# Optimization experiments

Measured on AMD Instinct MI355X. Metric: run time of the kernel, lower is better.

The kernel has to match this reference:

```python
import jax, jax.numpy as jnp
import numpy as np

EMBED_DIM = 256
NUM_HEADS = 4
HEAD_DIM = EMBED_DIM // NUM_HEADS  # 64
FEAT_X = FEAT_Y = 64               # 64*64 = 4096 tokens
THETA = 10000.0


def _axial_cos_sin(dim, end_x, end_y, theta):
    # compute_axial_cis: dim//4 frequencies per spatial axis, concatenated -> [N, dim//2]
    f = 1.0 / (theta ** (np.arange(0, dim, 4)[: dim // 4].astype(np.float32) / dim))
    t = np.arange(end_x * end_y)
    tx = (t % end_x).astype(np.float32)
    ty = (t // end_x).astype(np.float32)
    ang = np.concatenate([np.outer(tx, f), np.outer(ty, f)], axis=-1)  # [N, dim//2]
    return jnp.asarray(np.cos(ang)), jnp.asarray(np.sin(ang))


def _apply_rope(x, cos, sin):
    # x: [B, H, N, D]; adjacent pairs (x[..., 2i], x[..., 2i+1]) are the complex parts
    xr = x.reshape(*x.shape[:-1], -1, 2)
    xa, xb = xr[..., 0], xr[..., 1]          # [B, H, N, D//2]
    oa = xa * cos - xb * sin                  # cos/sin: [N, D//2], broadcast
    ob = xa * sin + xb * cos
    return jnp.stack([oa, ob], axis=-1).reshape(x.shape)


def setup_inputs() -> dict:
    key = jax.random.key(0)
    ks = jax.random.split(key, 8)
    B, N, D = 1, FEAT_X * FEAT_Y, EMBED_DIM
    s = 0.02  # weight init scale
    return {
        "q": jax.random.normal(ks[0], (B, N, D), jnp.float32),
        "k": jax.random.normal(ks[1], (B, N, D), jnp.float32),
        "v": jax.random.normal(ks[2], (B, N, D), jnp.float32),
        "wq": jax.random.normal(ks[3], (D, D), jnp.float32) * s,
        "bq": jnp.zeros((D,), jnp.float32),
        "wk": jax.random.normal(ks[4], (D, D), jnp.float32) * s,
        "bk": jnp.zeros((D,), jnp.float32),
        "wv": jax.random.normal(ks[5], (D, D), jnp.float32) * s,
        "bv": jnp.zeros((D,), jnp.float32),
        "wo": jax.random.normal(ks[6], (D, D), jnp.float32) * s,
        "bo": jnp.zeros((D,), jnp.float32),
        "return_attn": 0,
        "num_k_exclude_rope": 0,
    }


def reference(q, k, v, wq, bq, wk, bk, wv, bv, wo, bo, return_attn, num_k_exclude_rope):
    B, Nq, D = q.shape
    H, hd = NUM_HEADS, HEAD_DIM
    # QKV projections (weights stored [in, out], equiv to torch Linear W.T)
    qp = (q @ wq + bq).reshape(B, Nq, H, hd).transpose(0, 2, 1, 3)   # [B,H,Nq,hd]
    kp = (k @ wk + bk).reshape(B, -1, H, hd).transpose(0, 2, 1, 3)   # [B,H,Nk,hd]
    vp = (v @ wv + bv).reshape(B, -1, H, hd).transpose(0, 2, 1, 3)
    # rotary encoding on q and the first (Nk - num_k_exclude_rope) keys
    cos, sin = _axial_cos_sin(hd, FEAT_X, FEAT_Y, THETA)
    qp = _apply_rope(qp, cos, sin)
    nkr = kp.shape[2] - num_k_exclude_rope  # static Python int
    if num_k_exclude_rope > 0:
        kp = jnp.concatenate([_apply_rope(kp[:, :, :nkr], cos, sin), kp[:, :, nkr:]], axis=2)
    else:
        kp = _apply_rope(kp, cos, sin)
    # SDPA (eval: dropout_p = 0)
    scale = 1.0 / jnp.sqrt(jnp.asarray(hd, qp.dtype))
    scores = jnp.einsum("bhqd,bhkd->bhqk", qp, kp) * scale
    attn = jax.nn.softmax(scores, axis=-1)
    out = jnp.einsum("bhqk,bhkd->bhqd", attn, vp)
    out = out.transpose(0, 2, 1, 3).reshape(B, Nq, D)
    out = out @ wo + bo
    if return_attn:
        return out, scores  # attn_weight = q @ k^T * scale (pre-softmax, as in source)
    return out
```

## Files before the change

kernel.cpp:

```cpp
#include <hip/hip_runtime.h>
#include <hip/hip_bf16.h>
#include <math.h>

#define NTOK 4096
#define DEMB 256
#define NHEAD 4
#define HD 64

typedef short bf16x8 __attribute__((ext_vector_type(8)));
typedef short bf16x4 __attribute__((ext_vector_type(4)));
typedef float f32x4 __attribute__((ext_vector_type(4)));

__device__ __forceinline__ unsigned short f2b(float f) {
  union { float f; unsigned u; } v; v.f = f;
  return (unsigned short)((v.u + 0x7FFFu + ((v.u >> 16) & 1u)) >> 16);
}
__device__ __forceinline__ unsigned cvtpk(float lo, float hi) {
  unsigned r;
  asm("v_cvt_pk_bf16_f32 %0, %1, %2" : "=v"(r) : "v"(lo), "v"(hi));
  return r;
}

__global__ __launch_bounds__(256) void prep_kernel(
    const float* wq, const float* wk, const float* wv, const float* wo,
    unsigned short* wt, float2* cs) {
  int b = blockIdx.x;
  if (b < 64) {
    int m = b >> 4, tile = b & 15;
    int ti = tile >> 2, tj = tile & 3;
    const float* w = (m == 0) ? wq : (m == 1) ? wk : (m == 2) ? wv : wo;
    __shared__ float tl[64][65];
    int r = threadIdx.x >> 2, c4 = threadIdx.x & 3;
#pragma unroll
    for (int j = 0; j < 4; ++j) {
      float4 v4 = *(const float4*)(w + (ti * 64 + r) * 256 + tj * 64 + c4 * 16 + j * 4);
      tl[r][c4 * 16 + j * 4 + 0] = v4.x;
      tl[r][c4 * 16 + j * 4 + 1] = v4.y;
      tl[r][c4 * 16 + j * 4 + 2] = v4.z;
      tl[r][c4 * 16 + j * 4 + 3] = v4.w;
    }
    __syncthreads();
    unsigned short* dst = wt + m * 65536 + (tj * 64 + r) * 256 + ti * 64 + c4 * 16;
    bf16x8 o0, o1;
#pragma unroll
    for (int j = 0; j < 8; ++j) o0[j] = (short)f2b(tl[c4 * 16 + j][r]);
#pragma unroll
    for (int j = 0; j < 8; ++j) o1[j] = (short)f2b(tl[c4 * 16 + 8 + j][r]);
    *(bf16x8*)dst = o0;
    *(bf16x8*)(dst + 8) = o1;
  } else {
    int idx = (b - 64) * 256 + threadIdx.x;
    int n = idx >> 5, p = idx & 31;
    int j = p & 15;
    float f = powf(10000.0f, -(float)j / 16.0f);
    float ang = ((p < 16) ? (float)(n & 63) : (float)(n >> 6)) * f;
    cs[idx] = make_float2(cosf(ang), sinf(ang));
  }
}

__global__ __launch_bounds__(256) void qkvproj_kernel(
    const float* q, const float* k, const float* v, const unsigned short* wt,
    const float* bq, const float* bk, const float* bv, const float2* cs,
    unsigned short* qp, unsigned short* kp, unsigned short* vt) {
  int which = blockIdx.z;
  int wave = threadIdx.x >> 6, lane = threadIdx.x & 63;
  int col = lane & 15, g = lane >> 4;
  int mbase = blockIdx.x * 64 + wave * 16;
  int nbase = blockIdx.y * 64;
  const float* X = (which == 0) ? q : (which == 1) ? k : v;
  const unsigned short* W = wt + which * 65536;
  const float* bias = (which == 0) ? bq : (which == 1) ? bk : bv;

  f32x4 acc[4] = {};
  const float* ap0 = X + (mbase + col) * 256 + g * 8;
#pragma unroll
  for (int ks = 0; ks < 256; ks += 32) {
    float4 a0 = *(const float4*)(ap0 + ks);
    float4 a1 = *(const float4*)(ap0 + ks + 4);
    bf16x8 af;
    af[0] = (short)f2b(a0.x); af[1] = (short)f2b(a0.y);
    af[2] = (short)f2b(a0.z); af[3] = (short)f2b(a0.w);
    af[4] = (short)f2b(a1.x); af[5] = (short)f2b(a1.y);
    af[6] = (short)f2b(a1.z); af[7] = (short)f2b(a1.w);
#pragma unroll
    for (int nt = 0; nt < 4; ++nt) {
      bf16x8 bf_ = *(const bf16x8*)(W + (nbase + nt * 16 + col) * 256 + ks + g * 8);
      acc[nt] = __builtin_amdgcn_mfma_f32_16x16x32_bf16(af, bf_, acc[nt], 0, 0, 0);
    }
  }

  if (which == 2) {
    int kpos = ((mbase >> 5) << 5) + 8 * g + 4 * ((mbase >> 4) & 1);
#pragma unroll
    for (int nt = 0; nt < 4; ++nt) {
      int c = nbase + nt * 16 + col;
      float b = bias[c];
      bf16x4 pk;
#pragma unroll
      for (int r = 0; r < 4; ++r) pk[r] = (short)f2b(acc[nt][r] + b);
      *(bf16x4*)(vt + c * NTOK + kpos) = pk;
    }
  } else {
    const float QSC = 0.18033688f;
    unsigned short* dst = (which == 0) ? qp : kp;
#pragma unroll
    for (int nt = 0; nt < 4; ++nt) {
      int c = nbase + nt * 16 + col;
      float b = bias[c];
#pragma unroll
      for (int r = 0; r < 4; ++r) {
        int t = mbase + g * 4 + r;
        float val = acc[nt][r] + b;
        float2 csv = cs[t * 32 + ((c & 63) >> 1)];
        float pv = __shfl_xor(val, 1);
        float sn = (c & 1) ? csv.y : -csv.y;
        val = val * csv.x + pv * sn;
        if (which == 0) val *= QSC;
        dst[((c >> 6) * NTOK + t) * HD + (c & 63)] = f2b(val);
      }
    }
  }
}

__global__ __launch_bounds__(256, 4) void attn_kernel(
    const unsigned short* qp, const unsigned short* kp,
    const unsigned short* vt, unsigned short* pO, float* pml) {
  __shared__ alignas(16) unsigned char lds[32768];
  int id = blockIdx.x;
  int xcd = id & 7;
  int head = xcd >> 1;
  int rest = id >> 3;
  int qt128 = rest >> 2;
  int ks = (xcd & 1) * 4 + (rest & 3);
  int qb = qt128 * 128;
  int w = threadIdx.x >> 6, lane = threadIdx.x & 63;
  int col = lane & 15, g = lane >> 4;

  const unsigned short* kgp = kp + (head * NTOK + ks * 512) * HD;
  const unsigned short* vgp = vt + head * HD * NTOK + ks * 512;

  bf16x8 skr[2], svr[2];
  auto stage_issue = [&](int t) {
#pragma unroll
    for (int i = 0; i < 2; ++i) {
      int c = (int)threadIdx.x + i * 256, tok = c >> 3, part = c & 7;
      skr[i] = *(const bf16x8*)(kgp + (t * 64 + tok) * HD + part * 8);
      svr[i] = *(const bf16x8*)(vgp + tok * NTOK + t * 64 + part * 8);
    }
  };
  auto stage_write = [&](int buf) {
#pragma unroll
    for (int i = 0; i < 2; ++i) {
      int c = (int)threadIdx.x + i * 256, tok = c >> 3, part = c & 7;
      unsigned soff = (unsigned)(tok * 128) +
                      (unsigned)((part * 16) ^ ((tok & 7) << 4));
      *(bf16x8*)(lds + (unsigned)buf * 16384u + soff) = skr[i];
      *(bf16x8*)(lds + (unsigned)buf * 16384u + 8192u + soff) = svr[i];
    }
  };

  bf16x8 ones;
#pragma unroll
  for (int i = 0; i < 8; ++i) ones[i] = (short)0x3F80;

  bf16x8 qf[2][2];
  {
    const unsigned short* qr = qp + (head * NTOK + qb + w * 32) * HD;
#pragma unroll
    for (int qt = 0; qt < 2; ++qt)
#pragma unroll
      for (int h2 = 0; h2 < 2; ++h2)
        qf[qt][h2] = *(const bf16x8*)(qr + (qt * 16 + col) * HD + h2 * 32 + g * 8);
  }

  stage_issue(0);
  stage_write(0);
  stage_issue(1);
  __syncthreads();

  f32x4 acco[4][2] = {};
  f32x4 lacc[2] = {};

  for (int t = 0; t < 8; ++t) {
    int cur = t & 1;
    unsigned kb = (unsigned)cur * 16384u, vb = (unsigned)cur * 16384u + 8192u;

    f32x4 st[4][2] = {};
#pragma unroll
    for (int mt = 0; mt < 4; ++mt) {
      int tok = mt * 16 + col;
      unsigned ro = kb + (unsigned)(tok * 128) + (unsigned)((g * 16) ^ ((tok & 7) << 4));
      bf16x8 kf0 = *(const bf16x8*)(lds + ro);
      bf16x8 kf1 = *(const bf16x8*)(lds + (ro ^ 64u));
#pragma unroll
      for (int qt = 0; qt < 2; ++qt) {
        st[mt][qt] = __builtin_amdgcn_mfma_f32_16x16x32_bf16(kf0, qf[qt][0], st[mt][qt], 0, 0, 0);
        st[mt][qt] = __builtin_amdgcn_mfma_f32_16x16x32_bf16(kf1, qf[qt][1], st[mt][qt], 0, 0, 0);
      }
    }

    if (t < 7) {
      stage_write(cur ^ 1);
      if (t < 6) stage_issue(t + 2);
    }

    unsigned pw[2][2][4];
#pragma unroll
    for (int qt = 0; qt < 2; ++qt) {
      float p[4][4];
#pragma unroll
      for (int mt = 0; mt < 4; ++mt)
#pragma unroll
        for (int r = 0; r < 4; ++r) p[mt][r] = exp2f(st[mt][qt][r]);
#pragma unroll
      for (int kk = 0; kk < 2; ++kk) {
        pw[qt][kk][0] = cvtpk(p[2 * kk][0], p[2 * kk][1]);
        pw[qt][kk][1] = cvtpk(p[2 * kk][2], p[2 * kk][3]);
        pw[qt][kk][2] = cvtpk(p[2 * kk + 1][0], p[2 * kk + 1][1]);
        pw[qt][kk][3] = cvtpk(p[2 * kk + 1][2], p[2 * kk + 1][3]);
      }
    }

#pragma unroll
    for (int kk = 0; kk < 2; ++kk) {
      union { unsigned u[4]; bf16x8 v; } pf[2];
#pragma unroll
      for (int qt = 0; qt < 2; ++qt) {
        pf[qt].u[0] = pw[qt][kk][0]; pf[qt].u[1] = pw[qt][kk][1];
        pf[qt].u[2] = pw[qt][kk][2]; pf[qt].u[3] = pw[qt][kk][3];
        lacc[qt] = __builtin_amdgcn_mfma_f32_16x16x32_bf16(pf[qt].v, ones, lacc[qt], 0, 0, 0);
      }
#pragma unroll
      for (int nt = 0; nt < 4; ++nt) {
        int d = nt * 16 + col;
        unsigned off = vb + (unsigned)(d * 128) +
                       (unsigned)((kk * 64 + g * 16) ^ ((d & 7) << 4));
        bf16x8 vf = *(const bf16x8*)(lds + off);
#pragma unroll
        for (int qt = 0; qt < 2; ++qt)
          acco[nt][qt] = __builtin_amdgcn_mfma_f32_16x16x32_bf16(pf[qt].v, vf, acco[nt][qt], 0, 0, 0);
      }
    }
    __syncthreads();
  }

#pragma unroll
  for (int nt = 0; nt < 4; ++nt)
#pragma unroll
    for (int qt = 0; qt < 2; ++qt)
#pragma unroll
      for (int r = 0; r < 4; ++r) {
        int row = qb + w * 32 + qt * 16 + g * 4 + r;
        pO[((head * NTOK + row) * 8 + ks) * 64 + nt * 16 + col] =
            f2b(acco[nt][qt][r]);
      }
  if (col == 0) {
#pragma unroll
    for (int qt = 0; qt < 2; ++qt)
#pragma unroll
      for (int r = 0; r < 4; ++r) {
        int row = qb + w * 32 + qt * 16 + g * 4 + r;
        pml[(head * NTOK + row) * 8 + ks] = lacc[qt][r];
      }
  }
}

__global__ __launch_bounds__(256) void outproj_kernel(
    const unsigned short* pO, const float* pml, const unsigned short* wt_o,
    const float* bo, float* out) {
  __shared__ alignas(16) unsigned char attl[8192];
  int mbase = blockIdx.x * 16;
  int nbase = blockIdx.y * 128;
  int t = threadIdx.x;
  {
    int r = t >> 4, rest = t & 15;
    int h = rest >> 2, dq = rest & 3;
    int row = mbase + r;
    const float* mlp = pml + (h * NTOK + row) * 8;
    float den = 0.f;
#pragma unroll
    for (int ks = 0; ks < 8; ++ks) den += mlp[ks];
    float num[16] = {};
    const unsigned short* ob = pO + (h * NTOK + row) * 8 * 64 + dq * 16;
#pragma unroll
    for (int ks = 0; ks < 8; ++ks) {
      union { bf16x8 v; unsigned short s[8]; } a0, a1;
      a0.v = *(const bf16x8*)(ob + ks * 64);
      a1.v = *(const bf16x8*)(ob + ks * 64 + 8);
#pragma unroll
      for (int i = 0; i < 8; ++i) {
        num[i]     += __uint_as_float((unsigned)a0.s[i] << 16);
        num[8 + i] += __uint_as_float((unsigned)a1.s[i] << 16);
      }
    }
    float inv = 1.0f / den;
    union { unsigned short s[16]; bf16x8 v[2]; } ov;
#pragma unroll
    for (int i = 0; i < 16; ++i) ov.s[i] = f2b(num[i] * inv);
    unsigned base = (unsigned)(r * 512 + h * 128 + dq * 32);
    unsigned x = (unsigned)((r & 7) << 4);
    *(bf16x8*)(attl + (base ^ x)) = ov.v[0];
    *(bf16x8*)(attl + ((base + 16u) ^ x)) = ov.v[1];
  }
  __syncthreads();
  int w = t >> 6, lane = t & 63;
  int col = lane & 15, g = lane >> 4;
  f32x4 acc[2] = {};
#pragma unroll
  for (int ks = 0; ks < 256; ks += 32) {
    unsigned ab = (unsigned)(col * 512 + ks * 2 + g * 16) ^
                  (unsigned)((col & 7) << 4);
    bf16x8 af = *(const bf16x8*)(attl + ab);
#pragma unroll
    for (int ct = 0; ct < 2; ++ct) {
      bf16x8 bf_ = *(const bf16x8*)(wt_o + (nbase + w * 32 + ct * 16 + col) * 256 + ks + g * 8);
      acc[ct] = __builtin_amdgcn_mfma_f32_16x16x32_bf16(af, bf_, acc[ct], 0, 0, 0);
    }
  }
#pragma unroll
  for (int ct = 0; ct < 2; ++ct) {
    int c = nbase + w * 32 + ct * 16 + col;
    float b = bo[c];
#pragma unroll
    for (int r = 0; r < 4; ++r)
      out[(mbase + g * 4 + r) * 256 + c] = acc[ct][r] + b;
  }
}

extern "C" void kernel_launch(void* const* d_in, const int* in_sizes, int n_in,
                              void* d_out, int out_size, void* d_ws, size_t ws_size,
                              hipStream_t stream) {
  const float* q  = (const float*)d_in[0];
  const float* k  = (const float*)d_in[1];
  const float* v  = (const float*)d_in[2];
  const float* wq = (const float*)d_in[3];
  const float* bq = (const float*)d_in[4];
  const float* wk = (const float*)d_in[5];
  const float* bk = (const float*)d_in[6];
  const float* wv = (const float*)d_in[7];
  const float* bv = (const float*)d_in[8];
  const float* wo = (const float*)d_in[9];
  const float* bo = (const float*)d_in[10];
  float* out = (float*)d_out;

  char* ws = (char*)d_ws;
  float2* cs         = (float2*)ws;
  unsigned short* wt = (unsigned short*)(ws + (1u << 20));
  unsigned short* qp = (unsigned short*)(ws + 1536u * 1024u);
  unsigned short* kp = qp + NHEAD * NTOK * HD;
  unsigned short* vt = kp + NHEAD * NTOK * HD;
  unsigned short* pO = (unsigned short*)(ws + 9728u * 1024u);
  float* pml = (float*)(ws + 26624u * 1024u);

  prep_kernel<<<576, 256, 0, stream>>>(wq, wk, wv, wo, wt, cs);
  qkvproj_kernel<<<dim3(64, 4, 3), 256, 0, stream>>>(q, k, v, wt, bq, bk, bv, cs,
                                                     qp, kp, vt);
  attn_kernel<<<1024, 256, 0, stream>>>(qp, kp, vt, pO, pml);
  outproj_kernel<<<dim3(256, 2), 256, 0, stream>>>(pO, pml, wt + 3 * 65536, bo, out);
}
```

Measured before the change: 68.75 us.

## Double key splits in attention and halve projection column tiles for more parallelism

The attention kernel now splits keys into 16 chunks of 256 tokens instead of 8 chunks of 512. Each block uses half the shared memory and 32-token stages, and the launch grows to 2048 blocks with a higher occupancy bound. The V tile layout in shared memory is repacked to match. The QKV projection uses 32-column tiles with twice the grid, and the output projection now reduces 16 partial results per row. This adds wave-level parallelism and occupancy in exchange for twice the partial-output traffic and more reduction work in the output projection.

```diff
diff --git a/kernel.cpp b/kernel.cpp
--- a/kernel.cpp
+++ b/kernel.cpp
@@ -66,12 +66,12 @@
   int wave = threadIdx.x >> 6, lane = threadIdx.x & 63;
   int col = lane & 15, g = lane >> 4;
   int mbase = blockIdx.x * 64 + wave * 16;
-  int nbase = blockIdx.y * 64;
+  int nbase = blockIdx.y * 32;
   const float* X = (which == 0) ? q : (which == 1) ? k : v;
   const unsigned short* W = wt + which * 65536;
   const float* bias = (which == 0) ? bq : (which == 1) ? bk : bv;
 
-  f32x4 acc[4] = {};
+  f32x4 acc[2] = {};
   const float* ap0 = X + (mbase + col) * 256 + g * 8;
 #pragma unroll
   for (int ks = 0; ks < 256; ks += 32) {
@@ -83,7 +83,7 @@
     af[4] = (short)f2b(a1.x); af[5] = (short)f2b(a1.y);
     af[6] = (short)f2b(a1.z); af[7] = (short)f2b(a1.w);
 #pragma unroll
-    for (int nt = 0; nt < 4; ++nt) {
+    for (int nt = 0; nt < 2; ++nt) {
       bf16x8 bf_ = *(const bf16x8*)(W + (nbase + nt * 16 + col) * 256 + ks + g * 8);
       acc[nt] = __builtin_amdgcn_mfma_f32_16x16x32_bf16(af, bf_, acc[nt], 0, 0, 0);
     }
@@ -92,7 +92,7 @@
   if (which == 2) {
     int kpos = ((mbase >> 5) << 5) + 8 * g + 4 * ((mbase >> 4) & 1);
 #pragma unroll
-    for (int nt = 0; nt < 4; ++nt) {
+    for (int nt = 0; nt < 2; ++nt) {
       int c = nbase + nt * 16 + col;
       float b = bias[c];
       bf16x4 pk;
@@ -104,7 +104,7 @@
     const float QSC = 0.18033688f;
     unsigned short* dst = (which == 0) ? qp : kp;
 #pragma unroll
-    for (int nt = 0; nt < 4; ++nt) {
+    for (int nt = 0; nt < 2; ++nt) {
       int c = nbase + nt * 16 + col;
       float b = bias[c];
 #pragma unroll
@@ -122,41 +122,39 @@
   }
 }
 
-__global__ __launch_bounds__(256, 4) void attn_kernel(
+__global__ __launch_bounds__(256, 8) void attn_kernel(
     const unsigned short* qp, const unsigned short* kp,
     const unsigned short* vt, unsigned short* pO, float* pml) {
-  __shared__ alignas(16) unsigned char lds[32768];
+  __shared__ alignas(16) unsigned char lds[16384];
   int id = blockIdx.x;
   int xcd = id & 7;
   int head = xcd >> 1;
   int rest = id >> 3;
-  int qt128 = rest >> 2;
-  int ks = (xcd & 1) * 4 + (rest & 3);
+  int qt128 = rest >> 3;
+  int ks = (xcd & 1) * 8 + (rest & 7);
   int qb = qt128 * 128;
   int w = threadIdx.x >> 6, lane = threadIdx.x & 63;
   int col = lane & 15, g = lane >> 4;
-
-  const unsigned short* kgp = kp + (head * NTOK + ks * 512) * HD;
-  const unsigned short* vgp = vt + head * HD * NTOK + ks * 512;
-
-  bf16x8 skr[2], svr[2];
+  int tid = threadIdx.x;
+  int ktok = tid >> 3, kpart = tid & 7;
+  int vrow = tid >> 2, vpart = tid & 3;
+  unsigned soffk = (unsigned)(ktok * 128) +
+                   (unsigned)((kpart * 16) ^ ((ktok & 7) << 4));
+  unsigned soffv = (unsigned)((vrow >> 1) * 128) +
+                   (unsigned)((((vrow & 1) * 64) + vpart * 16) ^
+                              (((vrow >> 1) & 7) << 4));
+
+  const unsigned short* kgp = kp + (head * NTOK + ks * 256) * HD;
+  const unsigned short* vgp = vt + head * HD * NTOK + ks * 256;
+
+  bf16x8 skr, svr;
   auto stage_issue = [&](int t) {
-#pragma unroll
-    for (int i = 0; i < 2; ++i) {
-      int c = (int)threadIdx.x + i * 256, tok = c >> 3, part = c & 7;
-      skr[i] = *(const bf16x8*)(kgp + (t * 64 + tok) * HD + part * 8);
-      svr[i] = *(const bf16x8*)(vgp + tok * NTOK + t * 64 + part * 8);
-    }
+    skr = *(const bf16x8*)(kgp + (t * 32 + ktok) * HD + kpart * 8);
+    svr = *(const bf16x8*)(vgp + vrow * NTOK + t * 32 + vpart * 8);
   };
   auto stage_write = [&](int buf) {
-#pragma unroll
-    for (int i = 0; i < 2; ++i) {
-      int c = (int)threadIdx.x + i * 256, tok = c >> 3, part = c & 7;
-      unsigned soff = (unsigned)(tok * 128) +
-                      (unsigned)((part * 16) ^ ((tok & 7) << 4));
-      *(bf16x8*)(lds + (unsigned)buf * 16384u + soff) = skr[i];
-      *(bf16x8*)(lds + (unsigned)buf * 16384u + 8192u + soff) = svr[i];
-    }
+    *(bf16x8*)(lds + (unsigned)buf * 8192u + soffk) = skr;
+    *(bf16x8*)(lds + (unsigned)buf * 8192u + 4096u + soffv) = svr;
   };
 
   bf16x8 ones;
@@ -183,11 +181,11 @@
 
   for (int t = 0; t < 8; ++t) {
     int cur = t & 1;
-    unsigned kb = (unsigned)cur * 16384u, vb = (unsigned)cur * 16384u + 8192u;
-
-    f32x4 st[4][2] = {};
-#pragma unroll
-    for (int mt = 0; mt < 4; ++mt) {
+    unsigned kb = (unsigned)cur * 8192u, vb = kb + 4096u;
+
+    f32x4 st[2][2] = {};
+#pragma unroll
+    for (int mt = 0; mt < 2; ++mt) {
       int tok = mt * 16 + col;
       unsigned ro = kb + (unsigned)(tok * 128) + (unsigned)((g * 16) ^ ((tok & 7) << 4));
       bf16x8 kf0 = *(const bf16x8*)(lds + ro);
@@ -204,42 +202,36 @@
       if (t < 6) stage_issue(t + 2);
     }
 
-    unsigned pw[2][2][4];
+    unsigned pw[2][4];
 #pragma unroll
     for (int qt = 0; qt < 2; ++qt) {
-      float p[4][4];
-#pragma unroll
-      for (int mt = 0; mt < 4; ++mt)
+      float p[2][4];
+#pragma unroll
+      for (int mt = 0; mt < 2; ++mt)
 #pragma unroll
         for (int r = 0; r < 4; ++r) p[mt][r] = exp2f(st[mt][qt][r]);
-#pragma unroll
-      for (int kk = 0; kk < 2; ++kk) {
-        pw[qt][kk][0] = cvtpk(p[2 * kk][0], p[2 * kk][1]);
-        pw[qt][kk][1] = cvtpk(p[2 * kk][2], p[2 * kk][3]);
-        pw[qt][kk][2] = cvtpk(p[2 * kk + 1][0], p[2 * kk + 1][1]);
-        pw[qt][kk][3] = cvtpk(p[2 * kk + 1][2], p[2 * kk + 1][3]);
-      }
-    }
-
-#pragma unroll
-    for (int kk = 0; kk < 2; ++kk) {
-      union { unsigned u[4]; bf16x8 v; } pf[2];
-#pragma unroll
-      for (int qt = 0; qt < 2; ++qt) {
-        pf[qt].u[0] = pw[qt][kk][0]; pf[qt].u[1] = pw[qt][kk][1];
-        pf[qt].u[2] = pw[qt][kk][2]; pf[qt].u[3] = pw[qt][kk][3];
-        lacc[qt] = __builtin_amdgcn_mfma_f32_16x16x32_bf16(pf[qt].v, ones, lacc[qt], 0, 0, 0);
-      }
-#pragma unroll
-      for (int nt = 0; nt < 4; ++nt) {
-        int d = nt * 16 + col;
-        unsigned off = vb + (unsigned)(d * 128) +
-                       (unsigned)((kk * 64 + g * 16) ^ ((d & 7) << 4));
-        bf16x8 vf = *(const bf16x8*)(lds + off);
-#pragma unroll
-        for (int qt = 0; qt < 2; ++qt)
-          acco[nt][qt] = __builtin_amdgcn_mfma_f32_16x16x32_bf16(pf[qt].v, vf, acco[nt][qt], 0, 0, 0);
-      }
+      pw[qt][0] = cvtpk(p[0][0], p[0][1]);
+      pw[qt][1] = cvtpk(p[0][2], p[0][3]);
+      pw[qt][2] = cvtpk(p[1][0], p[1][1]);
+      pw[qt][3] = cvtpk(p[1][2], p[1][3]);
+    }
+
+    union { unsigned u[4]; bf16x8 v; } pf[2];
+#pragma unroll
+    for (int qt = 0; qt < 2; ++qt) {
+      pf[qt].u[0] = pw[qt][0]; pf[qt].u[1] = pw[qt][1];
+      pf[qt].u[2] = pw[qt][2]; pf[qt].u[3] = pw[qt][3];
+      lacc[qt] = __builtin_amdgcn_mfma_f32_16x16x32_bf16(pf[qt].v, ones, lacc[qt], 0, 0, 0);
+    }
+#pragma unroll
+    for (int nt = 0; nt < 4; ++nt) {
+      int d = nt * 16 + col;
+      unsigned voff = vb + (unsigned)((d >> 1) * 128) +
+                      (unsigned)((((d & 1) * 64) + g * 16) ^ (((d >> 1) & 7) << 4));
+      bf16x8 vf = *(const bf16x8*)(lds + voff);
+#pragma unroll
+      for (int qt = 0; qt < 2; ++qt)
+        acco[nt][qt] = __builtin_amdgcn_mfma_f32_16x16x32_bf16(pf[qt].v, vf, acco[nt][qt], 0, 0, 0);
     }
     __syncthreads();
   }
@@ -251,7 +243,7 @@
 #pragma unroll
       for (int r = 0; r < 4; ++r) {
         int row = qb + w * 32 + qt * 16 + g * 4 + r;
-        pO[((head * NTOK + row) * 8 + ks) * 64 + nt * 16 + col] =
+        pO[((head * NTOK + row) * 16 + ks) * 64 + nt * 16 + col] =
             f2b(acco[nt][qt][r]);
       }
   if (col == 0) {
@@ -260,7 +252,7 @@
 #pragma unroll
       for (int r = 0; r < 4; ++r) {
         int row = qb + w * 32 + qt * 16 + g * 4 + r;
-        pml[(head * NTOK + row) * 8 + ks] = lacc[qt][r];
+        pml[(head * NTOK + row) * 16 + ks] = lacc[qt][r];
       }
   }
 }
@@ -276,14 +268,14 @@
     int r = t >> 4, rest = t & 15;
     int h = rest >> 2, dq = rest & 3;
     int row = mbase + r;
-    const float* mlp = pml + (h * NTOK + row) * 8;
+    const float* mlp = pml + (h * NTOK + row) * 16;
     float den = 0.f;
 #pragma unroll
-    for (int ks = 0; ks < 8; ++ks) den += mlp[ks];
+    for (int ks = 0; ks < 16; ++ks) den += mlp[ks];
     float num[16] = {};
-    const unsigned short* ob = pO + (h * NTOK + row) * 8 * 64 + dq * 16;
-#pragma unroll
-    for (int ks = 0; ks < 8; ++ks) {
+    const unsigned short* ob = pO + (h * NTOK + row) * 16 * 64 + dq * 16;
+#pragma unroll
+    for (int ks = 0; ks < 16; ++ks) {
       union { bf16x8 v; unsigned short s[8]; } a0, a1;
       a0.v = *(const bf16x8*)(ob + ks * 64);
       a1.v = *(const bf16x8*)(ob + ks * 64 + 8);
@@ -349,12 +341,12 @@
   unsigned short* qp = (unsigned short*)(ws + 1536u * 1024u);
   unsigned short* kp = qp + NHEAD * NTOK * HD;
   unsigned short* vt = kp + NHEAD * NTOK * HD;
-  unsigned short* pO = (unsigned short*)(ws + 9728u * 1024u);
-  float* pml = (float*)(ws + 26624u * 1024u);
+  unsigned short* pO = (unsigned short*)(ws + 7680u * 1024u);
+  float* pml = (float*)(ws + 40960u * 1024u);
 
   prep_kernel<<<576, 256, 0, stream>>>(wq, wk, wv, wo, wt, cs);
-  qkvproj_kernel<<<dim3(64, 4, 3), 256, 0, stream>>>(q, k, v, wt, bq, bk, bv, cs,
+  qkvproj_kernel<<<dim3(64, 8, 3), 256, 0, stream>>>(q, k, v, wt, bq, bk, bv, cs,
                                                      qp, kp, vt);
-  attn_kernel<<<1024, 256, 0, stream>>>(qp, kp, vt, pO, pml);
+  attn_kernel<<<2048, 256, 0, stream>>>(qp, kp, vt, pO, pml);
   outproj_kernel<<<dim3(256, 2), 256, 0, stream>>>(pO, pml, wt + 3 * 65536, bo, out);
 }
```

Result: slower. 248.0 us (+260.7%).
